# Performance work log

Measured on AMD Instinct MI355X. Metric: run time of the kernel, lower is better.

## Reference

```python
import jax, jax.numpy as jnp
import numpy as np


def setup_inputs() -> dict:
    key = jax.random.key(0)
    k1, k2, k3 = jax.random.split(key, 3)
    B, S = 4096, 4096
    prediction = jax.random.normal(k1, (B, S), dtype=jnp.float32)
    target = jax.random.normal(k2, (B, S), dtype=jnp.float32)
    mask = jax.random.randint(k3, (B, S), 0, 2, dtype=jnp.int32)
    return {"prediction": prediction, "target": target, "mask": mask}


def reference(prediction, target, mask):
    # Masked MSE with ragged alignment: for each row, the j-th masked position
    # of `prediction` is compared against target[i, j] (i.e. target[:lens[i]]).
    m = mask != 0  # ignored_index == 0
    # rank of each masked position within its row -> index into target row
    rank = jnp.cumsum(m.astype(jnp.int32), axis=1) - 1  # [B, S]
    gathered_target = jnp.take_along_axis(target, jnp.clip(rank, 0, None), axis=1)
    diff2 = jnp.where(m, (prediction - gathered_target) ** 2, jnp.zeros((), prediction.dtype))
    return diff2.sum()  # reduction='sum'
```

## Files before the change

kernel.cpp:

```cpp
#include <hip/hip_runtime.h>

__device__ __forceinline__ int lanes_below(unsigned long long m) {
    return __builtin_amdgcn_mbcnt_hi((unsigned)(m >> 32),
           __builtin_amdgcn_mbcnt_lo((unsigned)m, 0u));
}

__global__ __launch_bounds__(512, 8) void masked_mse_rows(
    const float* __restrict__ pred,
    const float* __restrict__ target,
    const int*   __restrict__ mask,
    float*       __restrict__ row_sums,
    int S)
{
    const int tid  = threadIdx.x;
    const int lane = tid & 63;
    const int wid  = tid >> 6;
    const int row  = blockIdx.x;

    const float4* __restrict__ p4 = reinterpret_cast<const float4*>(pred + (size_t)row * S);
    const int4*   __restrict__ m4 = reinterpret_cast<const int4*>(mask + (size_t)row * S);
    const float*  __restrict__ trow = target + (size_t)row * S;

    const int4   ma = m4[tid];
    const int4   mb = m4[tid + 512];
    const float4 pa = p4[tid];
    const float4 pb = p4[tid + 512];

    const int c0 = (ma.x != 0), c1 = (ma.y != 0), c2 = (ma.z != 0), c3 = (ma.w != 0);
    const int c4 = (mb.x != 0), c5 = (mb.y != 0), c6 = (mb.z != 0), c7 = (mb.w != 0);

    const unsigned long long a0 = __ballot(c0);
    const unsigned long long a1 = __ballot(c1);
    const unsigned long long a2 = __ballot(c2);
    const unsigned long long a3 = __ballot(c3);
    const unsigned long long b0 = __ballot(c4);
    const unsigned long long b1 = __ballot(c5);
    const unsigned long long b2 = __ballot(c6);
    const unsigned long long b3 = __ballot(c7);

    const int pref_a = lanes_below(a0) + lanes_below(a1) + lanes_below(a2) + lanes_below(a3);
    const int pref_b = lanes_below(b0) + lanes_below(b1) + lanes_below(b2) + lanes_below(b3);
    const int tot_a  = __popcll(a0) + __popcll(a1) + __popcll(a2) + __popcll(a3);
    const int tot_b  = __popcll(b0) + __popcll(b1) + __popcll(b2) + __popcll(b3);

    __shared__ int   ta[8], tb[8];
    __shared__ float facc[8];
    if (lane == 0) { ta[wid] = tot_a; tb[wid] = tot_b; }
    __syncthreads();

    int woff_a = 0, base_b = 0, woff_b = 0;
    #pragma unroll
    for (int w = 0; w < 8; ++w) {
        woff_a += (w < wid) ? ta[w] : 0;
        base_b += ta[w];
        woff_b += (w < wid) ? tb[w] : 0;
    }

    int idx[8];
    {
        int r = woff_a + pref_a;
        idx[0] = r; r += c0;
        idx[1] = r; r += c1;
        idx[2] = r; r += c2;
        idx[3] = r; r += c3;
    }
    {
        int r = base_b + woff_b + pref_b;
        idx[4] = r; r += c4;
        idx[5] = r; r += c5;
        idx[6] = r; r += c6;
        idx[7] = r; r += c7;
    }
    float tv[8];
    #pragma unroll
    for (int j = 0; j < 8; ++j) tv[j] = trow[idx[j]];

    const float pv[8] = {pa.x, pa.y, pa.z, pa.w, pb.x, pb.y, pb.z, pb.w};
    const int   cs[8] = {c0, c1, c2, c3, c4, c5, c6, c7};
    float acc = 0.0f;
    #pragma unroll
    for (int j = 0; j < 8; ++j) {
        const float d = pv[j] - tv[j];
        acc += cs[j] ? d * d : 0.0f;
    }

    #pragma unroll
    for (int off = 32; off > 0; off >>= 1) acc += __shfl_down(acc, off, 64);
    if (lane == 0) facc[wid] = acc;
    __syncthreads();
    if (tid == 0) {
        float s = 0.0f;
        #pragma unroll
        for (int w = 0; w < 8; ++w) s += facc[w];
        row_sums[row] = s;
    }
}

__global__ __launch_bounds__(1024) void reduce_rows(
    const float* __restrict__ row_sums, float* __restrict__ out, int n)
{
    const int tid = threadIdx.x;
    float acc = 0.0f;
    const int n4 = n >> 2;
    const float4* rs4 = reinterpret_cast<const float4*>(row_sums);
    for (int i = tid; i < n4; i += 1024) {
        float4 v = rs4[i];
        acc += (v.x + v.y) + (v.z + v.w);
    }
    for (int i = (n4 << 2) + tid; i < n; i += 1024) acc += row_sums[i];

    #pragma unroll
    for (int off = 32; off > 0; off >>= 1) acc += __shfl_down(acc, off, 64);
    __shared__ float facc[16];
    if ((tid & 63) == 0) facc[tid >> 6] = acc;
    __syncthreads();
    if (tid == 0) {
        float s = 0.0f;
        #pragma unroll
        for (int w = 0; w < 16; ++w) s += facc[w];
        out[0] = s;
    }
}

extern "C" void kernel_launch(void* const* d_in, const int* in_sizes, int n_in,
                              void* d_out, int out_size, void* d_ws, size_t ws_size,
                              hipStream_t stream) {
    const float* pred   = (const float*)d_in[0];
    const float* target = (const float*)d_in[1];
    const int*   mask   = (const int*)d_in[2];
    float* out = (float*)d_out;
    float* row_sums = (float*)d_ws;

    const int S = 4096;
    const int B = in_sizes[0] / S;

    masked_mse_rows<<<B, 512, 0, stream>>>(pred, target, mask, row_sums, S);
    reduce_rows<<<1, 1024, 0, stream>>>(row_sums, out, B);
}
```

Measured before the change: 31.20 us.

## Compact masked predictions in LDS and read target contiguously; fuse reduction via atomics

Each block now scatters its masked prediction values into a compacted LDS buffer, then reads target with contiguous float4 loads and only up to the masked count. This replaces the per-element indirect gather from target and skips loading target past the row's masked total. The second reduce kernel is replaced by a memset plus one float atomicAdd per block. The cost is 16 KB of LDS per block, an extra barrier, and a non-deterministic summation order.

```diff
diff --git a/kernel.cpp b/kernel.cpp
--- a/kernel.cpp
+++ b/kernel.cpp
@@ -9,7 +9,7 @@
     const float* __restrict__ pred,
     const float* __restrict__ target,
     const int*   __restrict__ mask,
-    float*       __restrict__ row_sums,
+    float*       __restrict__ out,
     int S)
 {
     const int tid  = threadIdx.x;
@@ -20,6 +20,10 @@
     const float4* __restrict__ p4 = reinterpret_cast<const float4*>(pred + (size_t)row * S);
     const int4*   __restrict__ m4 = reinterpret_cast<const int4*>(mask + (size_t)row * S);
     const float*  __restrict__ trow = target + (size_t)row * S;
+
+    __shared__ __align__(16) float comp[4096];
+    __shared__ int   tsum[16];
+    __shared__ float facc[8];
 
     const int4   ma = m4[tid];
     const int4   mb = m4[tid + 512];
@@ -43,45 +47,54 @@
     const int tot_a  = __popcll(a0) + __popcll(a1) + __popcll(a2) + __popcll(a3);
     const int tot_b  = __popcll(b0) + __popcll(b1) + __popcll(b2) + __popcll(b3);
 
-    __shared__ int   ta[8], tb[8];
-    __shared__ float facc[8];
-    if (lane == 0) { ta[wid] = tot_a; tb[wid] = tot_b; }
+    if (lane == 0) { tsum[wid] = tot_a; tsum[8 + wid] = tot_b; }
     __syncthreads();
 
-    int woff_a = 0, base_b = 0, woff_b = 0;
+    int base_a = 0, pre_b = 0, sumA = 0, total = 0;
     #pragma unroll
     for (int w = 0; w < 8; ++w) {
-        woff_a += (w < wid) ? ta[w] : 0;
-        base_b += ta[w];
-        woff_b += (w < wid) ? tb[w] : 0;
+        const int va = tsum[w], vb = tsum[8 + w];
+        base_a += (w < wid) ? va : 0;
+        pre_b  += (w < wid) ? vb : 0;
+        sumA   += va;
+        total  += va + vb;
     }
+    const int base_b = sumA + pre_b;
 
-    int idx[8];
     {
-        int r = woff_a + pref_a;
-        idx[0] = r; r += c0;
-        idx[1] = r; r += c1;
-        idx[2] = r; r += c2;
-        idx[3] = r; r += c3;
+        int r = base_a + pref_a;
+        if (c0) { comp[r] = pa.x; ++r; }
+        if (c1) { comp[r] = pa.y; ++r; }
+        if (c2) { comp[r] = pa.z; ++r; }
+        if (c3) { comp[r] = pa.w; }
     }
     {
-        int r = base_b + woff_b + pref_b;
-        idx[4] = r; r += c4;
-        idx[5] = r; r += c5;
-        idx[6] = r; r += c6;
-        idx[7] = r; r += c7;
+        int r = base_b + pref_b;
+        if (c4) { comp[r] = pb.x; ++r; }
+        if (c5) { comp[r] = pb.y; ++r; }
+        if (c6) { comp[r] = pb.z; ++r; }
+        if (c7) { comp[r] = pb.w; }
     }
-    float tv[8];
-    #pragma unroll
-    for (int j = 0; j < 8; ++j) tv[j] = trow[idx[j]];
+    __syncthreads();
 
-    const float pv[8] = {pa.x, pa.y, pa.z, pa.w, pb.x, pb.y, pb.z, pb.w};
-    const int   cs[8] = {c0, c1, c2, c3, c4, c5, c6, c7};
     float acc = 0.0f;
-    #pragma unroll
-    for (int j = 0; j < 8; ++j) {
-        const float d = pv[j] - tv[j];
-        acc += cs[j] ? d * d : 0.0f;
+    const int k = total - 8 * tid;
+    if (k > 0) {
+        const float4* c4p = reinterpret_cast<const float4*>(comp);
+        const float4* t4p = reinterpret_cast<const float4*>(trow);
+        const float4 cv0 = c4p[2 * tid];
+        const float4 cv1 = c4p[2 * tid + 1];
+        const float4 tv0 = t4p[2 * tid];
+        const float4 tv1 = t4p[2 * tid + 1];
+        float d;
+        d = cv0.x - tv0.x; acc += (0 < k) ? d * d : 0.0f;
+        d = cv0.y - tv0.y; acc += (1 < k) ? d * d : 0.0f;
+        d = cv0.z - tv0.z; acc += (2 < k) ? d * d : 0.0f;
+        d = cv0.w - tv0.w; acc += (3 < k) ? d * d : 0.0f;
+        d = cv1.x - tv1.x; acc += (4 < k) ? d * d : 0.0f;
+        d = cv1.y - tv1.y; acc += (5 < k) ? d * d : 0.0f;
+        d = cv1.z - tv1.z; acc += (6 < k) ? d * d : 0.0f;
+        d = cv1.w - tv1.w; acc += (7 < k) ? d * d : 0.0f;
     }
 
     #pragma unroll
@@ -92,33 +105,7 @@
         float s = 0.0f;
         #pragma unroll
         for (int w = 0; w < 8; ++w) s += facc[w];
-        row_sums[row] = s;
-    }
-}
-
-__global__ __launch_bounds__(1024) void reduce_rows(
-    const float* __restrict__ row_sums, float* __restrict__ out, int n)
-{
-    const int tid = threadIdx.x;
-    float acc = 0.0f;
-    const int n4 = n >> 2;
-    const float4* rs4 = reinterpret_cast<const float4*>(row_sums);
-    for (int i = tid; i < n4; i += 1024) {
-        float4 v = rs4[i];
-        acc += (v.x + v.y) + (v.z + v.w);
-    }
-    for (int i = (n4 << 2) + tid; i < n; i += 1024) acc += row_sums[i];
-
-    #pragma unroll
-    for (int off = 32; off > 0; off >>= 1) acc += __shfl_down(acc, off, 64);
-    __shared__ float facc[16];
-    if ((tid & 63) == 0) facc[tid >> 6] = acc;
-    __syncthreads();
-    if (tid == 0) {
-        float s = 0.0f;
-        #pragma unroll
-        for (int w = 0; w < 16; ++w) s += facc[w];
-        out[0] = s;
+        atomicAdd(out, s);
     }
 }
 
@@ -129,11 +116,10 @@
     const float* target = (const float*)d_in[1];
     const int*   mask   = (const int*)d_in[2];
     float* out = (float*)d_out;
-    float* row_sums = (float*)d_ws;
 
     const int S = 4096;
     const int B = in_sizes[0] / S;
 
-    masked_mse_rows<<<B, 512, 0, stream>>>(pred, target, mask, row_sums, S);
-    reduce_rows<<<1, 1024, 0, stream>>>(row_sums, out, B);
+    hipMemsetAsync(out, 0, sizeof(float) * out_size, stream);
+    masked_mse_rows<<<B, 512, 0, stream>>>(pred, target, mask, out, S);
 }
```

New measurement: 69.30 us. +122.1%, slower.

## Fuse row and final reductions into one persistent cooperative kernel with grid sync

Applied to the files above, without the earlier changes.

Replaces the two-kernel scheme (one block per row, then a single-block reduction) with one cooperative kernel of 512 persistent blocks, each looping over several rows. A grid-wide sync then lets block 0 do the final reduction, removing the second launch and its gap. The cost is a grid barrier, a sequential per-block row loop with extra __syncthreads, and less memory-level parallelism per block, since each block handles one row at a time.

```diff
diff --git a/kernel.cpp b/kernel.cpp
--- a/kernel.cpp
+++ b/kernel.cpp
@@ -1,124 +1,134 @@
 #include <hip/hip_runtime.h>
+#include <hip/hip_cooperative_groups.h>
+
+namespace cg = cooperative_groups;
 
 __device__ __forceinline__ int lanes_below(unsigned long long m) {
     return __builtin_amdgcn_mbcnt_hi((unsigned)(m >> 32),
            __builtin_amdgcn_mbcnt_lo((unsigned)m, 0u));
 }
 
-__global__ __launch_bounds__(512, 8) void masked_mse_rows(
+__global__ __launch_bounds__(512, 8) void masked_mse_all(
     const float* __restrict__ pred,
     const float* __restrict__ target,
     const int*   __restrict__ mask,
     float*       __restrict__ row_sums,
-    int S)
+    float*       __restrict__ out,
+    int S, int B, int rows_per_block)
 {
     const int tid  = threadIdx.x;
     const int lane = tid & 63;
     const int wid  = tid >> 6;
-    const int row  = blockIdx.x;
 
-    const float4* __restrict__ p4 = reinterpret_cast<const float4*>(pred + (size_t)row * S);
-    const int4*   __restrict__ m4 = reinterpret_cast<const int4*>(mask + (size_t)row * S);
-    const float*  __restrict__ trow = target + (size_t)row * S;
+    __shared__ int   tsum[16];
+    __shared__ float facc[8];
 
-    const int4   ma = m4[tid];
-    const int4   mb = m4[tid + 512];
-    const float4 pa = p4[tid];
-    const float4 pb = p4[tid + 512];
+    for (int it = 0; it < rows_per_block; ++it) {
+        const int row = blockIdx.x + it * gridDim.x;
+        if (row < B) {
+            const float4* __restrict__ p4 = reinterpret_cast<const float4*>(pred + (size_t)row * S);
+            const int4*   __restrict__ m4 = reinterpret_cast<const int4*>(mask + (size_t)row * S);
+            const float*  __restrict__ trow = target + (size_t)row * S;
 
-    const int c0 = (ma.x != 0), c1 = (ma.y != 0), c2 = (ma.z != 0), c3 = (ma.w != 0);
-    const int c4 = (mb.x != 0), c5 = (mb.y != 0), c6 = (mb.z != 0), c7 = (mb.w != 0);
+            const int4   ma = m4[tid];
+            const int4   mb = m4[tid + 512];
+            const float4 pa = p4[tid];
+            const float4 pb = p4[tid + 512];
 
-    const unsigned long long a0 = __ballot(c0);
-    const unsigned long long a1 = __ballot(c1);
-    const unsigned long long a2 = __ballot(c2);
-    const unsigned long long a3 = __ballot(c3);
-    const unsigned long long b0 = __ballot(c4);
-    const unsigned long long b1 = __ballot(c5);
-    const unsigned long long b2 = __ballot(c6);
-    const unsigned long long b3 = __ballot(c7);
+            const int c0 = (ma.x != 0), c1 = (ma.y != 0), c2 = (ma.z != 0), c3 = (ma.w != 0);
+            const int c4 = (mb.x != 0), c5 = (mb.y != 0), c6 = (mb.z != 0), c7 = (mb.w != 0);
 
-    const int pref_a = lanes_below(a0) + lanes_below(a1) + lanes_below(a2) + lanes_below(a3);
-    const int pref_b = lanes_below(b0) + lanes_below(b1) + lanes_below(b2) + lanes_below(b3);
-    const int tot_a  = __popcll(a0) + __popcll(a1) + __popcll(a2) + __popcll(a3);
-    const int tot_b  = __popcll(b0) + __popcll(b1) + __popcll(b2) + __popcll(b3);
+            const unsigned long long a0 = __ballot(c0);
+            const unsigned long long a1 = __ballot(c1);
+            const unsigned long long a2 = __ballot(c2);
+            const unsigned long long a3 = __ballot(c3);
+            const unsigned long long b0 = __ballot(c4);
+            const unsigned long long b1 = __ballot(c5);
+            const unsigned long long b2 = __ballot(c6);
+            const unsigned long long b3 = __ballot(c7);
 
-    __shared__ int   ta[8], tb[8];
-    __shared__ float facc[8];
-    if (lane == 0) { ta[wid] = tot_a; tb[wid] = tot_b; }
-    __syncthreads();
+            const int pref_a = lanes_below(a0) + lanes_below(a1) + lanes_below(a2) + lanes_below(a3);
+            const int pref_b = lanes_below(b0) + lanes_below(b1) + lanes_below(b2) + lanes_below(b3);
+            const int tot_a  = __popcll(a0) + __popcll(a1) + __popcll(a2) + __popcll(a3);
+            const int tot_b  = __popcll(b0) + __popcll(b1) + __popcll(b2) + __popcll(b3);
 
-    int woff_a = 0, base_b = 0, woff_b = 0;
-    #pragma unroll
-    for (int w = 0; w < 8; ++w) {
-        woff_a += (w < wid) ? ta[w] : 0;
-        base_b += ta[w];
-        woff_b += (w < wid) ? tb[w] : 0;
+            if (lane == 0) { tsum[wid] = tot_a; tsum[8 + wid] = tot_b; }
+            __syncthreads();
+
+            int base_a = 0, pre_b = 0, sumA = 0;
+            #pragma unroll
+            for (int w = 0; w < 8; ++w) {
+                const int va = tsum[w], vb = tsum[8 + w];
+                base_a += (w < wid) ? va : 0;
+                pre_b  += (w < wid) ? vb : 0;
+                sumA   += va;
+            }
+            const int base_b = sumA + pre_b;
+
+            int idx[8];
+            {
+                int r = base_a + pref_a;
+                idx[0] = r; r += c0;
+                idx[1] = r; r += c1;
+                idx[2] = r; r += c2;
+                idx[3] = r; r += c3;
+            }
+            {
+                int r = base_b + pref_b;
+                idx[4] = r; r += c4;
+                idx[5] = r; r += c5;
+                idx[6] = r; r += c6;
+                idx[7] = r; r += c7;
+            }
+            float tv[8];
+            #pragma unroll
+            for (int j = 0; j < 8; ++j) tv[j] = trow[idx[j]];
+
+            const float pv[8] = {pa.x, pa.y, pa.z, pa.w, pb.x, pb.y, pb.z, pb.w};
+            const int   cs[8] = {c0, c1, c2, c3, c4, c5, c6, c7};
+            float acc = 0.0f;
+            #pragma unroll
+            for (int j = 0; j < 8; ++j) {
+                const float d = pv[j] - tv[j];
+                acc += cs[j] ? d * d : 0.0f;
+            }
+
+            #pragma unroll
+            for (int off = 32; off > 0; off >>= 1) acc += __shfl_down(acc, off, 64);
+            if (lane == 0) facc[wid] = acc;
+            __syncthreads();
+            if (tid == 0) {
+                float s = 0.0f;
+                #pragma unroll
+                for (int w = 0; w < 8; ++w) s += facc[w];
+                row_sums[row] = s;
+            }
+            __syncthreads();
+        }
     }
 
-    int idx[8];
-    {
-        int r = woff_a + pref_a;
-        idx[0] = r; r += c0;
-        idx[1] = r; r += c1;
-        idx[2] = r; r += c2;
-        idx[3] = r; r += c3;
-    }
-    {
-        int r = base_b + woff_b + pref_b;
-        idx[4] = r; r += c4;
-        idx[5] = r; r += c5;
-        idx[6] = r; r += c6;
-        idx[7] = r; r += c7;
-    }
-    float tv[8];
-    #pragma unroll
-    for (int j = 0; j < 8; ++j) tv[j] = trow[idx[j]];
+    cg::this_grid().sync();
 
-    const float pv[8] = {pa.x, pa.y, pa.z, pa.w, pb.x, pb.y, pb.z, pb.w};
-    const int   cs[8] = {c0, c1, c2, c3, c4, c5, c6, c7};
-    float acc = 0.0f;
-    #pragma unroll
-    for (int j = 0; j < 8; ++j) {
-        const float d = pv[j] - tv[j];
-        acc += cs[j] ? d * d : 0.0f;
-    }
+    if (blockIdx.x == 0) {
+        float acc = 0.0f;
+        const int n4 = B >> 2;
+        const float4* rs4 = reinterpret_cast<const float4*>(row_sums);
+        for (int i = tid; i < n4; i += 512) {
+            float4 v = rs4[i];
+            acc += (v.x + v.y) + (v.z + v.w);
+        }
+        for (int i = (n4 << 2) + tid; i < B; i += 512) acc += row_sums[i];
 
-    #pragma unroll
-    for (int off = 32; off > 0; off >>= 1) acc += __shfl_down(acc, off, 64);
-    if (lane == 0) facc[wid] = acc;
-    __syncthreads();
-    if (tid == 0) {
-        float s = 0.0f;
         #pragma unroll
-        for (int w = 0; w < 8; ++w) s += facc[w];
-        row_sums[row] = s;
-    }
-}
-
-__global__ __launch_bounds__(1024) void reduce_rows(
-    const float* __restrict__ row_sums, float* __restrict__ out, int n)
-{
-    const int tid = threadIdx.x;
-    float acc = 0.0f;
-    const int n4 = n >> 2;
-    const float4* rs4 = reinterpret_cast<const float4*>(row_sums);
-    for (int i = tid; i < n4; i += 1024) {
-        float4 v = rs4[i];
-        acc += (v.x + v.y) + (v.z + v.w);
-    }
-    for (int i = (n4 << 2) + tid; i < n; i += 1024) acc += row_sums[i];
-
-    #pragma unroll
-    for (int off = 32; off > 0; off >>= 1) acc += __shfl_down(acc, off, 64);
-    __shared__ float facc[16];
-    if ((tid & 63) == 0) facc[tid >> 6] = acc;
-    __syncthreads();
-    if (tid == 0) {
-        float s = 0.0f;
-        #pragma unroll
-        for (int w = 0; w < 16; ++w) s += facc[w];
-        out[0] = s;
+        for (int off = 32; off > 0; off >>= 1) acc += __shfl_down(acc, off, 64);
+        if (lane == 0) facc[wid] = acc;
+        __syncthreads();
+        if (tid == 0) {
+            float s = 0.0f;
+            #pragma unroll
+            for (int w = 0; w < 8; ++w) s += facc[w];
+            out[0] = s;
+        }
     }
 }
 
@@ -131,9 +141,14 @@
     float* out = (float*)d_out;
     float* row_sums = (float*)d_ws;
 
-    const int S = 4096;
-    const int B = in_sizes[0] / S;
+    int S = 4096;
+    int B = in_sizes[0] / S;
+    const int nblocks = 512;
+    int rows_per_block = (B + nblocks - 1) / nblocks;
 
-    masked_mse_rows<<<B, 512, 0, stream>>>(pred, target, mask, row_sums, S);
-    reduce_rows<<<1, 1024, 0, stream>>>(row_sums, out, B);
+    void* args[] = { (void*)&pred, (void*)&target, (void*)&mask,
+                     (void*)&row_sums, (void*)&out, (void*)&S, (void*)&B,
+                     (void*)&rows_per_block };
+    hipLaunchCooperativeKernel((void*)masked_mse_all, dim3(nblocks), dim3(512),
+                               args, 0, stream);
 }
```

After: 100.7 us. 223% more time.
